# Optimization experiments

Measured on AMD Instinct MI355X. Metric: run time of the kernel, lower is better.

The kernel has to match this reference:

```python
import jax, jax.numpy as jnp
import numpy as np

B, T, N = 16, 1024, 512        # batch, time tokens, neurons
DK_T, DK_S = 64, 128           # key dims (temporal, spatial)
# dim_T = N, dim_S = T, dim_value_T = N (required by cross einsum), heads = 1


def setup_inputs() -> dict:
    key = jax.random.key(0)
    ks = jax.random.split(key, 11)
    return {
        "x_T": jax.random.normal(ks[0], (B, T, N), jnp.float32),
        "x_S": jax.random.normal(ks[1], (B, N, T), jnp.float32),
        "Wq_T": jax.random.normal(ks[2], (N, DK_T), jnp.float32) * 0.05,
        "Wk_T": jax.random.normal(ks[3], (N, DK_T), jnp.float32) * 0.05,
        "Wv_T": jax.random.normal(ks[4], (N, N), jnp.float32) * 0.05,
        "Wq_S": jax.random.normal(ks[5], (T, DK_S), jnp.float32) * 0.05,
        "Wk_S": jax.random.normal(ks[6], (T, DK_S), jnp.float32) * 0.05,
        "Wout_T": jax.random.normal(ks[7], (N, N), jnp.float32) * 0.05,
        "bout_T": jax.random.normal(ks[8], (N,), jnp.float32) * 0.05,
        "bias_T": jax.random.normal(ks[9], (1, 1, 1, DK_T), jnp.float32),
        "bias_S": jax.random.normal(ks[10], (1, 1, 1, DK_S), jnp.float32),
    }


def reference(x_T, x_S, Wq_T, Wk_T, Wv_T, Wq_S, Wk_S, Wout_T, bout_T, bias_T, bias_S):
    scale_T = DK_T ** -0.5
    scale_S = DK_S ** -0.5
    # Temporal attention: tokens along time axis, heads=1 -> add h axis
    q_T = (x_T @ Wq_T)[:, None] * scale_T          # [b,1,t,dk_T]
    k_T = (x_T @ Wk_T)[:, None]                    # [b,1,t,dk_T]
    v_T = (x_T @ Wv_T)[:, None]                    # [b,1,t,n]  (dim_value_T = n)
    logits_T = jnp.einsum('bhid,bhjd->bhij', q_T + bias_T, k_T)  # [b,1,t,t]
    attn_T = jax.nn.softmax(logits_T, axis=-1)
    out_T = jnp.einsum('bhij,bhjd->bhid', attn_T, v_T)            # [b,1,t,n]
    # Spatial attention: tokens along neuron axis
    q_S = (x_S @ Wq_S)[:, None] * scale_S          # [b,1,n,dk_S]
    k_S = (x_S @ Wk_S)[:, None]                    # [b,1,n,dk_S]
    logits_S = jnp.einsum('bhid,bhjd->bhij', q_S + bias_S, k_S)   # [b,1,n,n]
    attn_S = jax.nn.softmax(logits_S, axis=-1)
    # spatial_temporal_1 cross combination: attn_S mixes the neuron axis of out_T
    out_T = jnp.einsum('bhij,bhtj->bhti', attn_S, out_T)          # [b,1,t,n]
    out_T = out_T.reshape(B, T, N)                 # 'b h t d -> b t (h d)'
    out_T = out_T @ Wout_T + bout_T                # to_out_T
    return jnp.transpose(out_T, (0, 2, 1))         # [b, n, t]
```

## Files before the change

### kernel.cpp

```cpp
#include <hip/hip_runtime.h>
#include <cstddef>

typedef short short8 __attribute__((ext_vector_type(8)));
typedef unsigned short ushortx8 __attribute__((ext_vector_type(8)));
typedef float floatx4 __attribute__((ext_vector_type(4)));

__device__ __forceinline__ unsigned int bf16_rne(float x) {
    unsigned int u = __float_as_uint(x);
    return (u + 0x7fffu + ((u >> 16) & 1u)) >> 16;
}

__device__ __forceinline__ void split4(const floatx4 v,
                                       unsigned long long& hp,
                                       unsigned long long& lp) {
    unsigned int h[4], l[4];
    #pragma unroll
    for (int j = 0; j < 4; ++j) {
        h[j] = bf16_rne(v[j]);
        float hf = __uint_as_float(h[j] << 16);
        l[j] = bf16_rne(v[j] - hf);
    }
    hp = (unsigned long long)(h[0] | (h[1] << 16)) |
         ((unsigned long long)(h[2] | (h[3] << 16)) << 32);
    lp = (unsigned long long)(l[0] | (l[1] << 16)) |
         ((unsigned long long)(l[2] | (l[3] << 16)) << 32);
}

__device__ __forceinline__ unsigned long long pack_hi4(const floatx4 v) {
    unsigned int h0 = bf16_rne(v[0]), h1 = bf16_rne(v[1]);
    unsigned int h2 = bf16_rne(v[2]), h3 = bf16_rne(v[3]);
    return (unsigned long long)(h0 | (h1 << 16)) |
           ((unsigned long long)(h2 | (h3 << 16)) << 32);
}

template<int BM, int BN, int AMODE, int BMODE, int OUTMODE, bool HASBIAS>
__global__ __launch_bounds__(256, 2)
void gemm_nt(const void* __restrict__ Ah_, const void* __restrict__ Al_,
             const void* __restrict__ Bh_, const void* __restrict__ Bl_,
             void* __restrict__ C_, void* __restrict__ Cl_,
             const float* __restrict__ bias,
             int K, int lda, int ldb, int ldc,
             long sA, long sB, long sC, float alpha, int nsplit)
{
    constexpr bool ALO = (AMODE == 1 || AMODE == 3);
    constexpr bool BLO = (BMODE == 1 || BMODE == 3);
    constexpr int LS = 40;
    __shared__ unsigned short Ash[2][BM][LS];
    __shared__ unsigned short Als[2][ALO ? BM : 1][LS];
    __shared__ unsigned short Bsh[2][BN][LS];
    __shared__ unsigned short Bls[2][BLO ? BN : 1][LS];

    const int b   = blockIdx.z;
    const int bm0 = blockIdx.y * BM;
    const int bn0 = blockIdx.x * BN;
    const int tid  = threadIdx.x;
    const int lane = tid & 63;
    const int wid  = tid >> 6;
    const int wr = wid >> 1, wc = wid & 1;
    constexpr int WM = BM / 2, WN = BN / 2;
    constexpr int FM = WM / 16, FN = WN / 16;
    floatx4 acc[FM][FN] = {};
    const int l15  = lane & 15;
    const int koff = (lane >> 4) * 8;

    constexpr int NAF = (AMODE <= 1) ? (BM * 32) / 1024 : 1;
    constexpr int NAH = (AMODE >= 2) ? (BM * 32) / 2048 : 1;
    constexpr int NBF = (BMODE <= 1) ? (BN * 32) / 1024 : 1;
    constexpr int NBH = (BMODE >= 2) ? (BN * 32) / 2048 : 1;
    floatx4  aF[NAF], bF[NBF];
    ushortx8 aH[NAH], aL[NAH], bH[NBH], bL[NBH];

    auto loadA = [&](int k0) {
        if (AMODE <= 1) {
            const float* A = (const float*)Ah_ + (long)b * sA;
            #pragma unroll
            for (int i = 0; i < NAF; ++i) {
                int flat = i * 1024 + tid * 4;
                int r = flat >> 5, c = flat & 31;
                aF[i] = *(const floatx4*)(A + (long)(bm0 + r) * lda + k0 + c);
            }
        } else {
            const unsigned short* A  = (const unsigned short*)Ah_ + (long)b * sA;
            const unsigned short* Al = (const unsigned short*)Al_ + (long)b * sA;
            #pragma unroll
            for (int i = 0; i < NAH; ++i) {
                int flat = i * 2048 + tid * 8;
                int r = flat >> 5, c = flat & 31;
                aH[i] = *(const ushortx8*)(A + (long)(bm0 + r) * lda + k0 + c);
                if (AMODE == 3)
                    aL[i] = *(const ushortx8*)(Al + (long)(bm0 + r) * lda + k0 + c);
            }
        }
    };
    auto loadB = [&](int k0) {
        if (BMODE <= 1) {
            const float* Bp = (const float*)Bh_ + (long)b * sB;
            #pragma unroll
            for (int i = 0; i < NBF; ++i) {
                int flat = i * 1024 + tid * 4;
                int r = flat >> 5, c = flat & 31;
                bF[i] = *(const floatx4*)(Bp + (long)(bn0 + r) * ldb + k0 + c);
            }
        } else {
            const unsigned short* Bp = (const unsigned short*)Bh_ + (long)b * sB;
            const unsigned short* Bl = (const unsigned short*)Bl_ + (long)b * sB;
            #pragma unroll
            for (int i = 0; i < NBH; ++i) {
                int flat = i * 2048 + tid * 8;
                int r = flat >> 5, c = flat & 31;
                bH[i] = *(const ushortx8*)(Bp + (long)(bn0 + r) * ldb + k0 + c);
                if (BMODE == 3)
                    bL[i] = *(const ushortx8*)(Bl + (long)(bn0 + r) * ldb + k0 + c);
            }
        }
    };
    auto writeA = [&](int bf) {
        if (AMODE <= 1) {
            #pragma unroll
            for (int i = 0; i < NAF; ++i) {
                int flat = i * 1024 + tid * 4;
                int r = flat >> 5, c = flat & 31;
                if (AMODE == 1) {
                    unsigned long long hp, lp; split4(aF[i], hp, lp);
                    *(unsigned long long*)&Ash[bf][r][c] = hp;
                    *(unsigned long long*)&Als[bf][r][c] = lp;
                } else {
                    *(unsigned long long*)&Ash[bf][r][c] = pack_hi4(aF[i]);
                }
            }
        } else {
            #pragma unroll
            for (int i = 0; i < NAH; ++i) {
                int flat = i * 2048 + tid * 8;
                int r = flat >> 5, c = flat & 31;
                *(ushortx8*)&Ash[bf][r][c] = aH[i];
                if (AMODE == 3) *(ushortx8*)&Als[bf][r][c] = aL[i];
            }
        }
    };
    auto writeB = [&](int bf) {
        if (BMODE <= 1) {
            #pragma unroll
            for (int i = 0; i < NBF; ++i) {
                int flat = i * 1024 + tid * 4;
                int r = flat >> 5, c = flat & 31;
                if (BMODE == 1) {
                    unsigned long long hp, lp; split4(bF[i], hp, lp);
                    *(unsigned long long*)&Bsh[bf][r][c] = hp;
                    *(unsigned long long*)&Bls[bf][r][c] = lp;
                } else {
                    *(unsigned long long*)&Bsh[bf][r][c] = pack_hi4(bF[i]);
                }
            }
        } else {
            #pragma unroll
            for (int i = 0; i < NBH; ++i) {
                int flat = i * 2048 + tid * 8;
                int r = flat >> 5, c = flat & 31;
                *(ushortx8*)&Bsh[bf][r][c] = bH[i];
                if (BMODE == 3) *(ushortx8*)&Bls[bf][r][c] = bL[i];
            }
        }
    };
    auto compute = [&](int bf) {
        short8 ah[FM], al[FM], bh[FN], bl[FN];
        #pragma unroll
        for (int mi = 0; mi < FM; ++mi) {
            ah[mi] = *(const short8*)&Ash[bf][wr * WM + mi * 16 + l15][koff];
            if (ALO) al[mi] = *(const short8*)&Als[bf][wr * WM + mi * 16 + l15][koff];
        }
        #pragma unroll
        for (int ni = 0; ni < FN; ++ni) {
            bh[ni] = *(const short8*)&Bsh[bf][wc * WN + ni * 16 + l15][koff];
            if (BLO) bl[ni] = *(const short8*)&Bls[bf][wc * WN + ni * 16 + l15][koff];
        }
        #pragma unroll
        for (int mi = 0; mi < FM; ++mi)
            #pragma unroll
            for (int ni = 0; ni < FN; ++ni) {
                if (ALO)
                    acc[mi][ni] = __builtin_amdgcn_mfma_f32_16x16x32_bf16(
                        al[mi], bh[ni], acc[mi][ni], 0, 0, 0);
                if (BLO)
                    acc[mi][ni] = __builtin_amdgcn_mfma_f32_16x16x32_bf16(
                        ah[mi], bl[ni], acc[mi][ni], 0, 0, 0);
                acc[mi][ni] = __builtin_amdgcn_mfma_f32_16x16x32_bf16(
                    ah[mi], bh[ni], acc[mi][ni], 0, 0, 0);
            }
    };

    loadA(0); loadB(0);
    writeA(0); writeB(0);
    __syncthreads();
    int cur = 0;
    for (int k0 = 32; k0 < K; k0 += 32) {
        loadA(k0); loadB(k0);
        compute(cur);
        writeA(cur ^ 1); writeB(cur ^ 1);
        __syncthreads();
        cur ^= 1;
    }
    compute(cur);

    const int rq = (lane >> 4) * 4;
    #pragma unroll
    for (int mi = 0; mi < FM; ++mi) {
        #pragma unroll
        for (int ni = 0; ni < FN; ++ni) {
            int gm = bm0 + wr * WM + mi * 16 + rq;
            int gn = bn0 + wc * WN + ni * 16 + l15;
            float ae = (gn < nsplit) ? alpha : 1.0f;
            float be = 0.f;
            if (HASBIAS) be = (gn < nsplit) ? bias[gn] : 0.0f;
            float vals[4];
            #pragma unroll
            for (int j = 0; j < 4; ++j) vals[j] = acc[mi][ni][j] * ae + be;
            if (OUTMODE == 0) {
                float* C = (float*)C_ + (long)b * sC;
                #pragma unroll
                for (int j = 0; j < 4; ++j) C[(long)(gm + j) * ldc + gn] = vals[j];
            } else if (OUTMODE == 1) {
                float* C = (float*)C_ + (long)b * sC;
                floatx4 o;
                #pragma unroll
                for (int j = 0; j < 4; ++j) o[j] = vals[j];
                *(floatx4*)(C + (long)gn * ldc + gm) = o;
            } else if (OUTMODE == 2) {
                unsigned short* Ch = (unsigned short*)C_ + (long)b * sC;
                unsigned short* Cl = (unsigned short*)Cl_ + (long)b * sC;
                #pragma unroll
                for (int j = 0; j < 4; ++j) {
                    unsigned int h = bf16_rne(vals[j]);
                    float hf = __uint_as_float(h << 16);
                    unsigned int lo = bf16_rne(vals[j] - hf);
                    Ch[(long)(gm + j) * ldc + gn] = (unsigned short)h;
                    Cl[(long)(gm + j) * ldc + gn] = (unsigned short)lo;
                }
            } else {
                unsigned short* Ch = (unsigned short*)C_ + (long)b * sC;
                #pragma unroll
                for (int j = 0; j < 4; ++j)
                    Ch[(long)(gm + j) * ldc + gn] = (unsigned short)bf16_rne(vals[j]);
            }
        }
    }
}

template<int COLS, int DK, int LDQK>
__global__ __launch_bounds__(256, 2)
void qk_softmax(const unsigned short* __restrict__ qk_h,
                const unsigned short* __restrict__ qk_l,
                unsigned short* __restrict__ P)
{
    constexpr int WCOLS = COLS / 4;
    constexpr int FN = WCOLS / 16;
    constexpr int QPAD = DK + 24;
    __shared__ unsigned short Qh[32][QPAD];
    __shared__ unsigned short Ql[32][QPAD];
    __shared__ float red[32][4];
    __shared__ unsigned short Pl[32][COLS + 8];

    const int b  = blockIdx.y;
    const int q0 = blockIdx.x * 32;
    const long rowBase = (long)b * COLS;
    const int tid = threadIdx.x;
    const int lane = tid & 63, wid = tid >> 6;
    const int l15 = lane & 15, g = lane >> 4;
    const int koff = g * 8;

    constexpr int QCH = DK / 8;
    for (int i = tid; i < 32 * QCH; i += 256) {
        int r = i / QCH, c = (i % QCH) * 8;
        *(ushortx8*)&Qh[r][c] = *(const ushortx8*)(qk_h + (rowBase + q0 + r) * LDQK + c);
        *(ushortx8*)&Ql[r][c] = *(const ushortx8*)(qk_l + (rowBase + q0 + r) * LDQK + c);
    }
    __syncthreads();

    floatx4 acc[2][FN] = {};
    const unsigned short* kh = qk_h + rowBase * LDQK + DK;
    const unsigned short* kl = qk_l + rowBase * LDQK + DK;

    #pragma unroll
    for (int kk = 0; kk < DK; kk += 32) {
        short8 ah[2], al[2];
        #pragma unroll
        for (int mi = 0; mi < 2; ++mi) {
            ah[mi] = *(const short8*)&Qh[mi * 16 + l15][kk + koff];
            al[mi] = *(const short8*)&Ql[mi * 16 + l15][kk + koff];
        }
        #pragma unroll
        for (int ni = 0; ni < FN; ++ni) {
            long krow = wid * WCOLS + ni * 16 + l15;
            short8 bh = *(const short8*)(kh + krow * LDQK + kk + koff);
            short8 bl = *(const short8*)(kl + krow * LDQK + kk + koff);
            #pragma unroll
            for (int mi = 0; mi < 2; ++mi) {
                acc[mi][ni] = __builtin_amdgcn_mfma_f32_16x16x32_bf16(al[mi], bh, acc[mi][ni], 0, 0, 0);
                acc[mi][ni] = __builtin_amdgcn_mfma_f32_16x16x32_bf16(ah[mi], bl, acc[mi][ni], 0, 0, 0);
                acc[mi][ni] = __builtin_amdgcn_mfma_f32_16x16x32_bf16(ah[mi], bh, acc[mi][ni], 0, 0, 0);
            }
        }
    }

    float pm[2][4];
    #pragma unroll
    for (int mi = 0; mi < 2; ++mi)
        #pragma unroll
        for (int j = 0; j < 4; ++j) {
            float m = acc[mi][0][j];
            #pragma unroll
            for (int ni = 1; ni < FN; ++ni) m = fmaxf(m, acc[mi][ni][j]);
            pm[mi][j] = m;
        }
    #pragma unroll
    for (int msk = 1; msk < 16; msk <<= 1) {
        #pragma unroll
        for (int mi = 0; mi < 2; ++mi)
            #pragma unroll
            for (int j = 0; j < 4; ++j)
                pm[mi][j] = fmaxf(pm[mi][j], __shfl_xor(pm[mi][j], msk));
    }
    if (l15 == 0) {
        #pragma unroll
        for (int mi = 0; mi < 2; ++mi)
            #pragma unroll
            for (int j = 0; j < 4; ++j) red[mi * 16 + g * 4 + j][wid] = pm[mi][j];
    }
    __syncthreads();
    float rm[2][4];
    #pragma unroll
    for (int mi = 0; mi < 2; ++mi)
        #pragma unroll
        for (int j = 0; j < 4; ++j) {
            const float* r4 = red[mi * 16 + g * 4 + j];
            rm[mi][j] = fmaxf(fmaxf(r4[0], r4[1]), fmaxf(r4[2], r4[3]));
        }
    __syncthreads();

    float ps[2][4] = {};
    #pragma unroll
    for (int mi = 0; mi < 2; ++mi)
        #pragma unroll
        for (int ni = 0; ni < FN; ++ni)
            #pragma unroll
            for (int j = 0; j < 4; ++j) {
                float e = __expf(acc[mi][ni][j] - rm[mi][j]);
                acc[mi][ni][j] = e;
                ps[mi][j] += e;
            }
    #pragma unroll
    for (int msk = 1; msk < 16; msk <<= 1) {
        #pragma unroll
        for (int mi = 0; mi < 2; ++mi)
            #pragma unroll
            for (int j = 0; j < 4; ++j)
                ps[mi][j] += __shfl_xor(ps[mi][j], msk);
    }
    if (l15 == 0) {
        #pragma unroll
        for (int mi = 0; mi < 2; ++mi)
            #pragma unroll
            for (int j = 0; j < 4; ++j) red[mi * 16 + g * 4 + j][wid] = ps[mi][j];
    }
    __syncthreads();
    float inv[2][4];
    #pragma unroll
    for (int mi = 0; mi < 2; ++mi)
        #pragma unroll
        for (int j = 0; j < 4; ++j) {
            const float* r4 = red[mi * 16 + g * 4 + j];
            inv[mi][j] = 1.0f / (r4[0] + r4[1] + r4[2] + r4[3]);
        }

    #pragma unroll
    for (int mi = 0; mi < 2; ++mi)
        #pragma unroll
        for (int ni = 0; ni < FN; ++ni)
            #pragma unroll
            for (int j = 0; j < 4; ++j)
                Pl[mi * 16 + g * 4 + j][wid * WCOLS + ni * 16 + l15] =
                    (unsigned short)bf16_rne(acc[mi][ni][j] * inv[mi][j]);
    __syncthreads();

    constexpr int PCH = COLS / 8;
    for (int i = tid; i < 32 * PCH; i += 256) {
        int r = i / PCH, c = (i % PCH) * 8;
        *(ushortx8*)(P + (rowBase + q0 + r) * COLS + c) = *(const ushortx8*)&Pl[r][c];
    }
}

__global__ __launch_bounds__(256)
void transpose_split(const float* __restrict__ in,
                     unsigned short* __restrict__ outH,
                     unsigned short* __restrict__ outL,
                     int R, int C, int rowOff, int ldo)
{
    __shared__ float tile[32][33];
    const int tc = blockIdx.x * 32, tr = blockIdx.y * 32;
    const int x = threadIdx.x, y = threadIdx.y;
    #pragma unroll
    for (int i = 0; i < 32; i += 8)
        tile[y + i][x] = in[(long)(tr + y + i) * C + tc + x];
    __syncthreads();
    #pragma unroll
    for (int i = 0; i < 32; i += 8) {
        float v = tile[x][y + i];
        unsigned int h = bf16_rne(v);
        float hf = __uint_as_float(h << 16);
        unsigned int lo = bf16_rne(v - hf);
        long idx = (long)(tc + y + i + rowOff) * ldo + tr + x;
        outH[idx] = (unsigned short)h;
        outL[idx] = (unsigned short)lo;
    }
}

extern "C" void kernel_launch(void* const* d_in, const int* in_sizes, int n_in,
                              void* d_out, int out_size, void* d_ws, size_t ws_size,
                              hipStream_t stream)
{
    (void)in_sizes; (void)n_in; (void)out_size; (void)ws_size;
    const float* x_T    = (const float*)d_in[0];
    const float* x_S    = (const float*)d_in[1];
    const float* Wq_T   = (const float*)d_in[2];
    const float* Wk_T   = (const float*)d_in[3];
    const float* Wv_T   = (const float*)d_in[4];
    const float* Wq_S   = (const float*)d_in[5];
    const float* Wk_S   = (const float*)d_in[6];
    const float* Wout_T = (const float*)d_in[7];
    const float* bout_T = (const float*)d_in[8];
    const float* bias_T = (const float*)d_in[9];
    const float* bias_S = (const float*)d_in[10];
    float* out = (float*)d_out;

    constexpr int B = 16, T = 1024, N = 512, DKT = 64, DKS = 128;
    typedef unsigned short us;

    char* w = (char*)d_ws;
    size_t off = 0;
    auto alloc = [&](size_t bytes) { char* p = w + off; off = (off + bytes + 255) & ~(size_t)255; return p; };
    us* wqkT_h = (us*)alloc(128 * 512 * 2);
    us* wqkT_l = (us*)alloc(128 * 512 * 2);
    us* wvt_h  = (us*)alloc(512 * 512 * 2);
    us* wvt_l  = (us*)alloc(512 * 512 * 2);
    us* wqks_h = (us*)alloc(256 * 1024 * 2);
    us* wqks_l = (us*)alloc(256 * 1024 * 2);
    us* wout_h = (us*)alloc(512 * 512 * 2);
    us* wout_l = (us*)alloc(512 * 512 * 2);
    us* qk_h   = (us*)alloc((size_t)16384 * 128 * 2);
    us* qk_l   = (us*)alloc((size_t)16384 * 128 * 2);
    us* P_T    = (us*)alloc((size_t)B * T * T * 2);
    us* P_S    = (us*)alloc((size_t)B * N * N * 2);
    us* vT_h   = (us*)alloc((size_t)B * N * T * 2);
    us* vT_l   = (us*)alloc((size_t)B * N * T * 2);
    us* outT_h = (us*)alloc((size_t)B * T * N * 2);
    us* outT_l = (us*)alloc((size_t)B * T * N * 2);
    us* out2_h = vT_h;
    us* out2_l = vT_l;

    const float scale_T = 0.125f;
    const float scale_S = 0.088388347648318447f;
    const int BIG = 1 << 30;

    dim3 tb(32, 8);
    transpose_split<<<dim3(2, 16),  tb, 0, stream>>>(Wq_T,   wqkT_h, wqkT_l, 512, 64,   0, 512);
    transpose_split<<<dim3(2, 16),  tb, 0, stream>>>(Wk_T,   wqkT_h, wqkT_l, 512, 64,  64, 512);
    transpose_split<<<dim3(16, 16), tb, 0, stream>>>(Wv_T,   wvt_h,  wvt_l,  512, 512,  0, 512);
    transpose_split<<<dim3(4, 32),  tb, 0, stream>>>(Wq_S,   wqks_h, wqks_l, 1024, 128, 0, 1024);
    transpose_split<<<dim3(4, 32),  tb, 0, stream>>>(Wk_S,   wqks_h, wqks_l, 1024, 128, 128, 1024);
    transpose_split<<<dim3(16, 16), tb, 0, stream>>>(Wout_T, wout_h, wout_l, 512, 512,  0, 512);

    gemm_nt<64, 64, 1, 3, 2, true><<<dim3(2, 256, 1), 256, 0, stream>>>(
        x_T, nullptr, wqkT_h, wqkT_l, qk_h, qk_l, bias_T,
        512, 512, 512, 128, 0, 0, 0, scale_T, 64);
    gemm_nt<128, 128, 3, 0, 3, false><<<dim3(8, 4, B), 256, 0, stream>>>(
        wvt_h, wvt_l, x_T, nullptr, vT_h, nullptr, nullptr,
        512, 512, 512, 1024, 0, (long)T * N, (long)N * T, 1.0f, 0);
    qk_softmax<1024, 64, 128><<<dim3(32, 16), 256, 0, stream>>>(qk_h, qk_l, P_T);
    gemm_nt<128, 128, 2, 2, 2, false><<<dim3(4, 8, B), 256, 0, stream>>>(
        P_T, nullptr, vT_h, nullptr, outT_h, outT_l, nullptr,
        1024, 1024, 1024, 512, (long)T * T, (long)N * T, (long)T * N, 1.0f, 0);

    gemm_nt<64, 64, 1, 3, 2, true><<<dim3(4, 128, 1), 256, 0, stream>>>(
        x_S, nullptr, wqks_h, wqks_l, qk_h, qk_l, bias_S,
        1024, 1024, 1024, 256, 0, 0, 0, scale_S, 128);
    qk_softmax<512, 128, 256><<<dim3(16, 16), 256, 0, stream>>>(qk_h, qk_l, P_S);
    gemm_nt<128, 128, 3, 2, 2, false><<<dim3(4, 8, B), 256, 0, stream>>>(
        outT_h, outT_l, P_S, nullptr, out2_h, out2_l, nullptr,
        512, 512, 512, 512, (long)T * N, (long)N * N, (long)T * N, 1.0f, 0);
    gemm_nt<128, 128, 3, 2, 1, true><<<dim3(4, 8, B), 256, 0, stream>>>(
        out2_h, out2_l, wout_h, nullptr, out, nullptr, bout_T,
        512, 512, 512, 1024, (long)T * N, 0, (long)N * T, 1.0f, BIG);
}
```

Measured before the change: 236.7 us.

## Remap GEMM workgroups per XCD and use 32x128 tiles for QK projections

Workgroup IDs in the batched GEMM are remapped so consecutive tiles land on the same XCD of the MI355X, which is meant to improve L2 reuse of shared A/B panels. Loader loops are generalized to handle tiles whose chunk count is not a multiple of 256 threads. The Q/K projection GEMMs switch from 64x64 to 32x128 tiles so each block reads the full projected width at once, cutting redundant reads of the large x input. Smaller BM gives less MFMA work per warp and adds a predicated partial load.

```diff
diff --git a/kernel.cpp b/kernel.cpp
--- a/kernel.cpp
+++ b/kernel.cpp
@@ -50,9 +50,18 @@
     __shared__ unsigned short Bsh[2][BN][LS];
     __shared__ unsigned short Bls[2][BLO ? BN : 1][LS];
 
+    const unsigned int gx = gridDim.x;
+    const unsigned int nwg = gx * gridDim.y;
+    unsigned int flat = blockIdx.y * gx + blockIdx.x;
+    {
+        unsigned int qq = nwg >> 3, rr = nwg & 7;
+        unsigned int xcd = flat & 7, idx = flat >> 3;
+        flat = (xcd < rr) ? (xcd * (qq + 1) + idx)
+                          : (rr * (qq + 1) + (xcd - rr) * qq + idx);
+    }
     const int b   = blockIdx.z;
-    const int bm0 = blockIdx.y * BM;
-    const int bn0 = blockIdx.x * BN;
+    const int bm0 = (flat / gx) * BM;
+    const int bn0 = (flat % gx) * BN;
     const int tid  = threadIdx.x;
     const int lane = tid & 63;
     const int wid  = tid >> 6;
@@ -63,10 +72,14 @@
     const int l15  = lane & 15;
     const int koff = (lane >> 4) * 8;
 
-    constexpr int NAF = (AMODE <= 1) ? (BM * 32) / 1024 : 1;
-    constexpr int NAH = (AMODE >= 2) ? (BM * 32) / 2048 : 1;
-    constexpr int NBF = (BMODE <= 1) ? (BN * 32) / 1024 : 1;
-    constexpr int NBH = (BMODE >= 2) ? (BN * 32) / 2048 : 1;
+    constexpr int ACHF = BM * 32 / 4, NAF0 = (ACHF + 255) / 256;
+    constexpr int ACHH = BM * 32 / 8, NAH0 = (ACHH + 255) / 256;
+    constexpr int BCHF = BN * 32 / 4, NBF0 = (BCHF + 255) / 256;
+    constexpr int BCHH = BN * 32 / 8, NBH0 = (BCHH + 255) / 256;
+    constexpr int NAF = (AMODE <= 1) ? NAF0 : 1;
+    constexpr int NAH = (AMODE >= 2) ? NAH0 : 1;
+    constexpr int NBF = (BMODE <= 1) ? NBF0 : 1;
+    constexpr int NBH = (BMODE >= 2) ? NBH0 : 1;
     floatx4  aF[NAF], bF[NBF];
     ushortx8 aH[NAH], aL[NAH], bH[NBH], bL[NBH];
 
@@ -75,20 +88,26 @@
             const float* A = (const float*)Ah_ + (long)b * sA;
             #pragma unroll
             for (int i = 0; i < NAF; ++i) {
-                int flat = i * 1024 + tid * 4;
-                int r = flat >> 5, c = flat & 31;
-                aF[i] = *(const floatx4*)(A + (long)(bm0 + r) * lda + k0 + c);
+                int idx = i * 256 + tid;
+                if (ACHF % 256 == 0 || idx < ACHF) {
+                    int flatc = idx * 4;
+                    int r = flatc >> 5, c = flatc & 31;
+                    aF[i] = *(const floatx4*)(A + (long)(bm0 + r) * lda + k0 + c);
+                }
             }
         } else {
             const unsigned short* A  = (const unsigned short*)Ah_ + (long)b * sA;
             const unsigned short* Al = (const unsigned short*)Al_ + (long)b * sA;
             #pragma unroll
             for (int i = 0; i < NAH; ++i) {
-                int flat = i * 2048 + tid * 8;
-                int r = flat >> 5, c = flat & 31;
-                aH[i] = *(const ushortx8*)(A + (long)(bm0 + r) * lda + k0 + c);
-                if (AMODE == 3)
-                    aL[i] = *(const ushortx8*)(Al + (long)(bm0 + r) * lda + k0 + c);
+                int idx = i * 256 + tid;
+                if (ACHH % 256 == 0 || idx < ACHH) {
+                    int flatc = idx * 8;
+                    int r = flatc >> 5, c = flatc & 31;
+                    aH[i] = *(const ushortx8*)(A + (long)(bm0 + r) * lda + k0 + c);
+                    if (AMODE == 3)
+                        aL[i] = *(const ushortx8*)(Al + (long)(bm0 + r) * lda + k0 + c);
+                }
             }
         }
     };
@@ -97,20 +116,26 @@
             const float* Bp = (const float*)Bh_ + (long)b * sB;
             #pragma unroll
             for (int i = 0; i < NBF; ++i) {
-                int flat = i * 1024 + tid * 4;
-                int r = flat >> 5, c = flat & 31;
-                bF[i] = *(const floatx4*)(Bp + (long)(bn0 + r) * ldb + k0 + c);
+                int idx = i * 256 + tid;
+                if (BCHF % 256 == 0 || idx < BCHF) {
+                    int flatc = idx * 4;
+                    int r = flatc >> 5, c = flatc & 31;
+                    bF[i] = *(const floatx4*)(Bp + (long)(bn0 + r) * ldb + k0 + c);
+                }
             }
         } else {
             const unsigned short* Bp = (const unsigned short*)Bh_ + (long)b * sB;
             const unsigned short* Bl = (const unsigned short*)Bl_ + (long)b * sB;
             #pragma unroll
             for (int i = 0; i < NBH; ++i) {
-                int flat = i * 2048 + tid * 8;
-                int r = flat >> 5, c = flat & 31;
-                bH[i] = *(const ushortx8*)(Bp + (long)(bn0 + r) * ldb + k0 + c);
-                if (BMODE == 3)
-                    bL[i] = *(const ushortx8*)(Bl + (long)(bn0 + r) * ldb + k0 + c);
+                int idx = i * 256 + tid;
+                if (BCHH % 256 == 0 || idx < BCHH) {
+                    int flatc = idx * 8;
+                    int r = flatc >> 5, c = flatc & 31;
+                    bH[i] = *(const ushortx8*)(Bp + (long)(bn0 + r) * ldb + k0 + c);
+                    if (BMODE == 3)
+                        bL[i] = *(const ushortx8*)(Bl + (long)(bn0 + r) * ldb + k0 + c);
+                }
             }
         }
     };
@@ -118,23 +143,29 @@
         if (AMODE <= 1) {
             #pragma unroll
             for (int i = 0; i < NAF; ++i) {
-                int flat = i * 1024 + tid * 4;
-                int r = flat >> 5, c = flat & 31;
-                if (AMODE == 1) {
-                    unsigned long long hp, lp; split4(aF[i], hp, lp);
-                    *(unsigned long long*)&Ash[bf][r][c] = hp;
-                    *(unsigned long long*)&Als[bf][r][c] = lp;
-                } else {
-                    *(unsigned long long*)&Ash[bf][r][c] = pack_hi4(aF[i]);
+                int idx = i * 256 + tid;
+                if (ACHF % 256 == 0 || idx < ACHF) {
+                    int flatc = idx * 4;
+                    int r = flatc >> 5, c = flatc & 31;
+                    if (AMODE == 1) {
+                        unsigned long long hp, lp; split4(aF[i], hp, lp);
+                        *(unsigned long long*)&Ash[bf][r][c] = hp;
+                        *(unsigned long long*)&Als[bf][r][c] = lp;
+                    } else {
+                        *(unsigned long long*)&Ash[bf][r][c] = pack_hi4(aF[i]);
+                    }
                 }
             }
         } else {
             #pragma unroll
             for (int i = 0; i < NAH; ++i) {
-                int flat = i * 2048 + tid * 8;
-                int r = flat >> 5, c = flat & 31;
-                *(ushortx8*)&Ash[bf][r][c] = aH[i];
-                if (AMODE == 3) *(ushortx8*)&Als[bf][r][c] = aL[i];
+                int idx = i * 256 + tid;
+                if (ACHH % 256 == 0 || idx < ACHH) {
+                    int flatc = idx * 8;
+                    int r = flatc >> 5, c = flatc & 31;
+                    *(ushortx8*)&Ash[bf][r][c] = aH[i];
+                    if (AMODE == 3) *(ushortx8*)&Als[bf][r][c] = aL[i];
+                }
             }
         }
     };
@@ -142,23 +173,29 @@
         if (BMODE <= 1) {
             #pragma unroll
             for (int i = 0; i < NBF; ++i) {
-                int flat = i * 1024 + tid * 4;
-                int r = flat >> 5, c = flat & 31;
-                if (BMODE == 1) {
-                    unsigned long long hp, lp; split4(bF[i], hp, lp);
-                    *(unsigned long long*)&Bsh[bf][r][c] = hp;
-                    *(unsigned long long*)&Bls[bf][r][c] = lp;
-                } else {
-                    *(unsigned long long*)&Bsh[bf][r][c] = pack_hi4(bF[i]);
+                int idx = i * 256 + tid;
+                if (BCHF % 256 == 0 || idx < BCHF) {
+                    int flatc = idx * 4;
+                    int r = flatc >> 5, c = flatc & 31;
+                    if (BMODE == 1) {
+                        unsigned long long hp, lp; split4(bF[i], hp, lp);
+                        *(unsigned long long*)&Bsh[bf][r][c] = hp;
+                        *(unsigned long long*)&Bls[bf][r][c] = lp;
+                    } else {
+                        *(unsigned long long*)&Bsh[bf][r][c] = pack_hi4(bF[i]);
+                    }
                 }
             }
         } else {
             #pragma unroll
             for (int i = 0; i < NBH; ++i) {
-                int flat = i * 2048 + tid * 8;
-                int r = flat >> 5, c = flat & 31;
-                *(ushortx8*)&Bsh[bf][r][c] = bH[i];
-                if (BMODE == 3) *(ushortx8*)&Bls[bf][r][c] = bL[i];
+                int idx = i * 256 + tid;
+                if (BCHH % 256 == 0 || idx < BCHH) {
+                    int flatc = idx * 8;
+                    int r = flatc >> 5, c = flatc & 31;
+                    *(ushortx8*)&Bsh[bf][r][c] = bH[i];
+                    if (BMODE == 3) *(ushortx8*)&Bls[bf][r][c] = bL[i];
+                }
             }
         }
     };
@@ -469,7 +506,7 @@
     transpose_split<<<dim3(4, 32),  tb, 0, stream>>>(Wk_S,   wqks_h, wqks_l, 1024, 128, 128, 1024);
     transpose_split<<<dim3(16, 16), tb, 0, stream>>>(Wout_T, wout_h, wout_l, 512, 512,  0, 512);
 
-    gemm_nt<64, 64, 1, 3, 2, true><<<dim3(2, 256, 1), 256, 0, stream>>>(
+    gemm_nt<32, 128, 1, 3, 2, true><<<dim3(1, 512, 1), 256, 0, stream>>>(
         x_T, nullptr, wqkT_h, wqkT_l, qk_h, qk_l, bias_T,
         512, 512, 512, 128, 0, 0, 0, scale_T, 64);
     gemm_nt<128, 128, 3, 0, 3, false><<<dim3(8, 4, B), 256, 0, stream>>>(
@@ -480,7 +517,7 @@
         P_T, nullptr, vT_h, nullptr, outT_h, outT_l, nullptr,
         1024, 1024, 1024, 512, (long)T * T, (long)N * T, (long)T * N, 1.0f, 0);
 
-    gemm_nt<64, 64, 1, 3, 2, true><<<dim3(4, 128, 1), 256, 0, stream>>>(
+    gemm_nt<32, 128, 1, 3, 2, true><<<dim3(2, 256, 1), 256, 0, stream>>>(
         x_S, nullptr, wqks_h, wqks_l, qk_h, qk_l, bias_S,
         1024, 1024, 1024, 256, 0, 0, 0, scale_S, 128);
     qk_softmax<512, 128, 256><<<dim3(16, 16), 256, 0, stream>>>(qk_h, qk_l, P_S);
```

New measurement: 221.8 us. 6.3% less time.
